# Optimization experiments

Measured on AMD Instinct MI355X. Metric: run time of the kernel, lower is better.

Reference implementation:

```python
import jax, jax.numpy as jnp
import numpy as np

B, N, G, M = 16, 8192, 512, 32
ENC = 384   # encoder_dims
TRD = 384   # trans_dim (must equal ENC due to cls-pos concat)
EPS = 1e-5


def _fps(xyz, n_samples):
    # farthest point sampling: xyz [B,N,3] -> idx [B,n_samples] int32
    b, n, _ = xyz.shape
    def body(carry, _):
        dists, farthest = carry                       # [B,N], [B]
        centroid = jnp.take_along_axis(xyz, farthest[:, None, None], axis=1)  # [B,1,3]
        d = jnp.sum((xyz - centroid) ** 2, -1)        # [B,N]
        dists = jnp.minimum(dists, d)
        nxt = jnp.argmax(dists, -1).astype(jnp.int32)
        return (dists, nxt), farthest
    init = (jnp.full((b, n), 1e10, xyz.dtype), jnp.zeros((b,), jnp.int32))
    _, idxs = jax.lax.scan(body, init, None, length=n_samples)
    return idxs.T                                     # [B,n_samples]


def _group(pts):
    # FPS centers + kNN neighborhoods, neighborhood recentered on its center
    fps_idx = _fps(pts, G)                                    # [B,G]
    center = jax.vmap(lambda p, i: p[i])(pts, fps_idx)        # [B,G,3]
    d2 = jnp.sum((center[:, :, None, :] - pts[:, None, :, :]) ** 2, -1)  # [B,G,N]
    _, knn_idx = jax.lax.top_k(-d2, M)                        # [B,G,M]
    nbhd = jax.vmap(lambda p, i: p[i])(pts, knn_idx)          # [B,G,M,3]
    nbhd = nbhd - center[:, :, None, :]
    return nbhd, center


def _bn(x, g, b, m, v):
    return (x - m) * jax.lax.rsqrt(v + EPS) * g + b


def _forward(pts, W1, b1, g1, be1, m1, v1, W2, b2,
             W3, b3, g2, be2, m2, v2, W4, b4,
             Wp1, bp1, Wp2, bp2, cls_pos):
    nbhd, center = _group(pts)                                # [B,G,M,3], [B,G,3]
    # Encoder (Point-MAE, BN in eval mode)
    f = jnp.einsum('bgmc,cd->bgmd', nbhd, W1) + b1            # [B,G,M,128]
    f = jax.nn.relu(_bn(f, g1, be1, m1, v1))
    f = jnp.einsum('bgmc,cd->bgmd', f, W2) + b2               # [B,G,M,256]
    fg = jnp.max(f, axis=2, keepdims=True)                    # [B,G,1,256]
    f = jnp.concatenate([jnp.broadcast_to(fg, f.shape), f], -1)  # [B,G,M,512]
    f = jnp.einsum('bgmc,cd->bgmd', f, W3) + b3
    f = jax.nn.relu(_bn(f, g2, be2, m2, v2))
    f = jnp.einsum('bgmc,cd->bgmd', f, W4) + b4               # [B,G,M,ENC]
    x = jnp.max(f, axis=2)                                    # [B,G,ENC]
    # pos embed MLP on centers
    pos = jax.nn.gelu(center @ Wp1 + bp1) @ Wp2 + bp2         # [B,G,TRD]
    cls = jnp.broadcast_to(cls_pos, (pts.shape[0], 1, ENC))
    pos = jnp.concatenate([cls, pos], axis=1)                 # [B,G+1,TRD]
    return x, pos


def setup_inputs() -> dict:
    key = jax.random.key(0)
    ks = jax.random.split(key, 20)
    nrm = lambda k, s, sc: jax.random.normal(k, s, jnp.float32) * sc
    uni = lambda k, s: jax.random.uniform(k, s, jnp.float32, 0.5, 1.5)
    return {
        'pts': jax.random.normal(ks[0], (B, N, 3), jnp.float32),
        'W1': nrm(ks[1], (3, 128), 0.1), 'b1': jnp.zeros((128,), jnp.float32),
        'g1': uni(ks[2], (128,)), 'be1': nrm(ks[3], (128,), 0.1),
        'm1': nrm(ks[4], (128,), 0.1), 'v1': uni(ks[5], (128,)),
        'W2': nrm(ks[6], (128, 256), 0.05), 'b2': jnp.zeros((256,), jnp.float32),
        'W3': nrm(ks[7], (512, 512), 0.04), 'b3': jnp.zeros((512,), jnp.float32),
        'g2': uni(ks[8], (512,)), 'be2': nrm(ks[9], (512,), 0.1),
        'm2': nrm(ks[10], (512,), 0.1), 'v2': uni(ks[11], (512,)),
        'W4': nrm(ks[12], (512, ENC), 0.04), 'b4': jnp.zeros((ENC,), jnp.float32),
        'Wp1': nrm(ks[13], (3, 128), 0.1), 'bp1': jnp.zeros((128,), jnp.float32),
        'Wp2': nrm(ks[14], (128, TRD), 0.08), 'bp2': jnp.zeros((TRD,), jnp.float32),
        'cls_pos': nrm(ks[15], (1, 1, ENC), 0.02),
    }


def reference(pts, W1, b1, g1, be1, m1, v1, W2, b2, W3, b3, g2, be2, m2, v2,
              W4, b4, Wp1, bp1, Wp2, bp2, cls_pos):
    return _forward(pts, W1, b1, g1, be1, m1, v1, W2, b2, W3, b3, g2, be2,
                    m2, v2, W4, b4, Wp1, bp1, Wp2, bp2, cls_pos)
```

## Files before the change

### kernel.cpp

```cpp
#include <hip/hip_runtime.h>

typedef _Float16 f16;
typedef _Float16 f16x8 __attribute__((ext_vector_type(8)));
typedef float    f32x4 __attribute__((ext_vector_type(4)));
typedef float    f32x2 __attribute__((ext_vector_type(2)));

#define NB   16
#define NP   8192
#define NG   512
#define NM   32
#define ENC  384
#define NROWS (NB * NG * NM)

__device__ __forceinline__ void gl_lds16(const void* g, void* l) {
  __builtin_amdgcn_global_load_lds((const __attribute__((address_space(1))) unsigned int*)g,
                                   (__attribute__((address_space(3))) unsigned int*)l, 16, 0, 0);
}

__device__ __forceinline__ f32x2 pk_add(f32x2 a, f32x2 b) {
  f32x2 d;
  asm("v_pk_add_f32 %0, %1, %2" : "=v"(d) : "v"(a), "v"(b));
  return d;
}
__device__ __forceinline__ f32x2 pk_mul(f32x2 a, f32x2 b) {
  f32x2 d;
  asm("v_pk_mul_f32 %0, %1, %2" : "=v"(d) : "v"(a), "v"(b));
  return d;
}

__device__ __forceinline__ unsigned long long kmax(unsigned long long a, unsigned long long b) {
  return a > b ? a : b;
}
__device__ __forceinline__ unsigned long long kmin(unsigned long long a, unsigned long long b) {
  return a < b ? a : b;
}

template <int CTRL>
__device__ __forceinline__ unsigned long long dpp_kmax(unsigned long long k) {
  int lo = (int)(unsigned)(k & 0xFFFFFFFFull);
  int hi = (int)(unsigned)(k >> 32);
  int olo = __builtin_amdgcn_update_dpp(lo, lo, CTRL, 0xF, 0xF, false);
  int ohi = __builtin_amdgcn_update_dpp(hi, hi, CTRL, 0xF, 0xF, false);
  unsigned long long o = ((unsigned long long)(unsigned)ohi << 32) | (unsigned)olo;
  return kmax(k, o);
}
template <int CTRL>
__device__ __forceinline__ unsigned long long dpp_kmin(unsigned long long k) {
  int lo = (int)(unsigned)(k & 0xFFFFFFFFull);
  int hi = (int)(unsigned)(k >> 32);
  int olo = __builtin_amdgcn_update_dpp(lo, lo, CTRL, 0xF, 0xF, false);
  int ohi = __builtin_amdgcn_update_dpp(hi, hi, CTRL, 0xF, 0xF, false);
  unsigned long long o = ((unsigned long long)(unsigned)ohi << 32) | (unsigned)olo;
  return kmin(k, o);
}
__device__ __forceinline__ unsigned long long swz16_kmax(unsigned long long k) {
  int lo = (int)(unsigned)(k & 0xFFFFFFFFull);
  int hi = (int)(unsigned)(k >> 32);
  int olo = __builtin_amdgcn_ds_swizzle(lo, 0x401F);
  int ohi = __builtin_amdgcn_ds_swizzle(hi, 0x401F);
  unsigned long long o = ((unsigned long long)(unsigned)ohi << 32) | (unsigned)olo;
  return kmax(k, o);
}
__device__ __forceinline__ unsigned long long swz16_kmin(unsigned long long k) {
  int lo = (int)(unsigned)(k & 0xFFFFFFFFull);
  int hi = (int)(unsigned)(k >> 32);
  int olo = __builtin_amdgcn_ds_swizzle(lo, 0x401F);
  int ohi = __builtin_amdgcn_ds_swizzle(hi, 0x401F);
  unsigned long long o = ((unsigned long long)(unsigned)ohi << 32) | (unsigned)olo;
  return kmin(k, o);
}

#define DPP_QUAD_XOR1 0xB1
#define DPP_QUAD_XOR2 0x4E
#define DPP_HALF_MIRR 0x141
#define DPP_ROW_MIRR  0x140

__global__ __launch_bounds__(512) void fps_kernel(const float* __restrict__ pts,
                                                  float* __restrict__ centers) {
#pragma clang fp contract(off)
  const int b = blockIdx.x;
  const float* pb = pts + (size_t)b * NP * 3;
  const int t = threadIdx.x;
  const int lane = t & 63, wid = t >> 6;
  __shared__ float spx[NP], spy[NP], spz[NP];
  __shared__ unsigned long long swk[2][16];
  f32x2 px2[8], py2[8], pz2[8];
  float dd[16];
#pragma unroll
  for (int i = 0; i < 16; ++i) {
    int idx = t + i * 512;
    float x = pb[idx * 3 + 0], y = pb[idx * 3 + 1], z = pb[idx * 3 + 2];
    px2[i >> 1][i & 1] = x; py2[i >> 1][i & 1] = y; pz2[i >> 1][i & 1] = z;
    dd[i] = 1e10f;
    spx[idx] = x; spy[idx] = y; spz[idx] = z;
  }
  __syncthreads();
  float cx = spx[0], cy = spy[0], cz = spz[0];
  for (int g = 0; g < NG; ++g) {
    if (t == 0) {
      float* c = centers + ((size_t)b * NG + g) * 3;
      c[0] = cx; c[1] = cy; c[2] = cz;
    }
    f32x2 ncx = {-cx, -cx}, ncy = {-cy, -cy}, ncz = {-cz, -cz};
    float best = -1.0f; int bslot = 0;
#pragma unroll
    for (int p = 0; p < 8; ++p) {
      f32x2 dx = pk_add(px2[p], ncx);
      f32x2 dy = pk_add(py2[p], ncy);
      f32x2 dz = pk_add(pz2[p], ncz);
      f32x2 d2 = pk_add(pk_add(pk_mul(dx, dx), pk_mul(dy, dy)), pk_mul(dz, dz));
      dd[2 * p] = fminf(dd[2 * p], d2[0]);
      if (dd[2 * p] > best) { best = dd[2 * p]; bslot = 2 * p; }
      dd[2 * p + 1] = fminf(dd[2 * p + 1], d2[1]);
      if (dd[2 * p + 1] > best) { best = dd[2 * p + 1]; bslot = 2 * p + 1; }
    }
    int bidx = t + bslot * 512;
    unsigned long long key =
        ((unsigned long long)__float_as_uint(best) << 13) | (unsigned)(8191 - bidx);
    key = dpp_kmax<DPP_QUAD_XOR1>(key);
    key = dpp_kmax<DPP_QUAD_XOR2>(key);
    key = dpp_kmax<DPP_HALF_MIRR>(key);
    key = dpp_kmax<DPP_ROW_MIRR>(key);
    key = swz16_kmax(key);
    const int p = g & 1;
    if ((lane & 31) == 0) swk[p][wid * 2 + (lane >> 5)] = key;
    __syncthreads();
    unsigned long long k2 = swk[p][lane & 15];
    k2 = dpp_kmax<DPP_QUAD_XOR1>(k2);
    k2 = dpp_kmax<DPP_QUAD_XOR2>(k2);
    k2 = dpp_kmax<DPP_HALF_MIRR>(k2);
    k2 = dpp_kmax<DPP_ROW_MIRR>(k2);
    int widx = 8191 - (int)(k2 & 0x1FFFull);
    cx = spx[widx]; cy = spy[widx]; cz = spz[widx];
  }
}

__global__ __launch_bounds__(256) void knn_kernel(const float* __restrict__ pts,
                                                  const float* __restrict__ centers,
                                                  int* __restrict__ knn_idx) {
#pragma clang fp contract(off)
  const int gg = blockIdx.x;
  const int b = gg >> 9;
  const float* pb = pts + (size_t)b * NP * 3;
  const float* c = centers + (size_t)gg * 3;
  const float cx = c[0], cy = c[1], cz = c[2];
  __shared__ unsigned long long swk[2][8];
  const int t = threadIdx.x, lane = t & 63, wid = t >> 6;
  float d[32];
  float lmin = 3e38f; int lidx = 0;
#pragma unroll
  for (int i = 0; i < 32; ++i) {
    int idx = i * 256 + t;
    float dx = __fsub_rn(cx, pb[idx * 3 + 0]);
    float dy = __fsub_rn(cy, pb[idx * 3 + 1]);
    float dz = __fsub_rn(cz, pb[idx * 3 + 2]);
    d[i] = __fadd_rn(__fadd_rn(__fmul_rn(dx, dx), __fmul_rn(dy, dy)), __fmul_rn(dz, dz));
    if (d[i] < lmin) { lmin = d[i]; lidx = idx; }
  }
  int* outp = knn_idx + (size_t)gg * NM;
  for (int r = 0; r < NM; ++r) {
    unsigned long long key =
        ((unsigned long long)__float_as_uint(lmin) << 13) | (unsigned)lidx;
    key = dpp_kmin<DPP_QUAD_XOR1>(key);
    key = dpp_kmin<DPP_QUAD_XOR2>(key);
    key = dpp_kmin<DPP_HALF_MIRR>(key);
    key = dpp_kmin<DPP_ROW_MIRR>(key);
    key = swz16_kmin(key);
    const int p = r & 1;
    if ((lane & 31) == 0) swk[p][wid * 2 + (lane >> 5)] = key;
    __syncthreads();
    unsigned long long k2 = swk[p][lane & 7];
    k2 = dpp_kmin<DPP_QUAD_XOR1>(k2);
    k2 = dpp_kmin<DPP_QUAD_XOR2>(k2);
    k2 = dpp_kmin<DPP_HALF_MIRR>(k2);
    int i0 = (int)(k2 & 0x1FFFull);
    if (t == 0) outp[r] = i0;
    if ((i0 & 255) == t) {
      int slot = i0 >> 8;
      lmin = 3e38f; lidx = 0;
#pragma unroll
      for (int i = 0; i < 32; ++i) {
        float di = (i == slot) ? 3e38f : d[i];
        d[i] = di;
        if (di < lmin) { lmin = di; lidx = i * 256 + t; }
      }
    }
  }
}

__global__ void quant_kernel(const float* __restrict__ W2, const float* __restrict__ W3,
                             const float* __restrict__ W4, const float* __restrict__ Wp2,
                             const float* __restrict__ b1, const float* __restrict__ g1,
                             const float* __restrict__ be1, const float* __restrict__ m1,
                             const float* __restrict__ v1, const float* __restrict__ g2,
                             const float* __restrict__ be2, const float* __restrict__ m2,
                             const float* __restrict__ v2,
                             f16* __restrict__ W2T, f16* __restrict__ W3aT,
                             f16* __restrict__ W3bT, f16* __restrict__ W4T,
                             f16* __restrict__ Wp2T,
                             float* __restrict__ s1, float* __restrict__ sh1,
                             float* __restrict__ s2, float* __restrict__ sh2) {
  int i = blockIdx.x * 256 + threadIdx.x;
  if (i < 32768) { int n = i >> 7, k = i & 127; W2T[i] = (f16)W2[(size_t)k * 256 + n]; return; }
  i -= 32768;
  if (i < 131072) { int n = i >> 8, k = i & 255; W3aT[i] = (f16)W3[(size_t)k * 512 + n]; return; }
  i -= 131072;
  if (i < 131072) { int n = i >> 8, k = i & 255; W3bT[i] = (f16)W3[(size_t)(256 + k) * 512 + n]; return; }
  i -= 131072;
  if (i < 196608) { int n = i >> 9, k = i & 511; W4T[i] = (f16)W4[(size_t)k * 384 + n]; return; }
  i -= 196608;
  if (i < 49152) { int n = i >> 7, k = i & 127; Wp2T[i] = (f16)Wp2[(size_t)k * 384 + n]; return; }
  i -= 49152;
  if (i < 128) {
    float s = g1[i] * rsqrtf(v1[i] + 1e-5f);
    s1[i] = s; sh1[i] = (b1[i] - m1[i]) * s + be1[i];
    return;
  }
  i -= 128;
  if (i < 512) {
    float s = g2[i] * rsqrtf(v2[i] + 1e-5f);
    s2[i] = s; sh2[i] = be2[i] - m2[i] * s;
    return;
  }
}

template <int WRITE_F2>
__global__ __launch_bounds__(256) void l2f_kernel(const float* __restrict__ pts,
                                                  const float* __restrict__ centers,
                                                  const int* __restrict__ knn_idx,
                                                  const float* __restrict__ W1,
                                                  const float* __restrict__ s1,
                                                  const float* __restrict__ sh1,
                                                  const f16* __restrict__ W2T,
                                                  const float* __restrict__ b2,
                                                  f16* __restrict__ fg,
                                                  f16* __restrict__ f2, int grow0) {
  __shared__ __align__(16) f16 sF1[128 * 128];
  __shared__ float snb[128][3];
  const int t = threadIdx.x, lane = t & 63, wid = t >> 6;
  const int wr = wid >> 1, wc = wid & 1;
  const int l15 = lane & 15, lhi = lane >> 4;
  const int grow = grow0 + blockIdx.x * 128;
  const int y = blockIdx.y;

  if (t < 128) {
    int row = grow + t;
    int gg = row >> 5;
    int b = gg >> 9;
    int idx = knn_idx[(size_t)gg * NM + (row & 31)];
    const float* p = pts + ((size_t)b * NP + idx) * 3;
    const float* c = centers + (size_t)gg * 3;
    snb[t][0] = p[0] - c[0];
    snb[t][1] = p[1] - c[1];
    snb[t][2] = p[2] - c[2];
  }
  __syncthreads();
  {
    int row = t >> 1, c0 = (t & 1) * 64;
    float nx = snb[row][0], ny = snb[row][1], nz = snb[row][2];
    int sw = (row & 7) << 4;
#pragma unroll
    for (int cc = 0; cc < 64; cc += 8) {
      f16x8 v;
#pragma unroll
      for (int j = 0; j < 8; ++j) {
        int c = c0 + cc + j;
        float a = nx * W1[c] + ny * W1[128 + c] + nz * W1[256 + c];
        a = a * s1[c] + sh1[c];
        v[j] = (f16)fmaxf(a, 0.0f);
      }
      *(f16x8*)((char*)sF1 + row * 256 + (((c0 + cc) * 2) ^ sw)) = v;
    }
  }
  __syncthreads();

  f32x4 acc[4][4];
#pragma unroll
  for (int m = 0; m < 4; ++m)
#pragma unroll
    for (int n = 0; n < 4; ++n) acc[m][n] = (f32x4){0.f, 0.f, 0.f, 0.f};

  const f16* Wb = W2T + (size_t)(y * 128) * 128;
#pragma unroll
  for (int ks = 0; ks < 4; ++ks) {
    f16x8 af[4], bf[4];
#pragma unroll
    for (int m = 0; m < 4; ++m) {
      int row = wr * 64 + m * 16 + l15;
      af[m] = *(const f16x8*)((const char*)sF1 + row * 256 + ((ks * 64 + lhi * 16) ^ ((row & 7) << 4)));
    }
#pragma unroll
    for (int n = 0; n < 4; ++n) {
      int nr = wc * 64 + n * 16 + l15;
      bf[n] = *(const f16x8*)(Wb + (size_t)nr * 128 + ks * 32 + lhi * 8);
    }
#pragma unroll
    for (int m = 0; m < 4; ++m)
#pragma unroll
      for (int n = 0; n < 4; ++n)
        acc[m][n] = __builtin_amdgcn_mfma_f32_16x16x32_f16(af[m], bf[n], acc[m][n], 0, 0, 0);
  }

  float bias[4];
#pragma unroll
  for (int n = 0; n < 4; ++n) bias[n] = b2[y * 128 + wc * 64 + n * 16 + l15];
#pragma unroll
  for (int p = 0; p < 2; ++p) {
#pragma unroll
    for (int n = 0; n < 4; ++n) {
      float v = acc[2 * p][n][0];
#pragma unroll
      for (int i = 1; i < 4; ++i) v = fmaxf(v, acc[2 * p][n][i]);
#pragma unroll
      for (int i = 0; i < 4; ++i) v = fmaxf(v, acc[2 * p + 1][n][i]);
      v = fmaxf(v, __shfl_xor(v, 16));
      v = fmaxf(v, __shfl_xor(v, 32));
      if (lhi == 0)
        fg[(size_t)((grow >> 5) + wr * 2 + p) * 256 + y * 128 + wc * 64 + n * 16 + l15] =
            (f16)(v + bias[n]);
    }
  }

  if (WRITE_F2) {
    __syncthreads();
    f16* sF2 = sF1;
#pragma unroll
    for (int n = 0; n < 4; ++n) {
      int col = wc * 64 + n * 16 + l15;
#pragma unroll
      for (int m = 0; m < 4; ++m)
#pragma unroll
        for (int i = 0; i < 4; ++i) {
          int row = wr * 64 + m * 16 + lhi * 4 + i;
          sF2[row * 128 + col] = (f16)(acc[m][n][i] + bias[n]);
        }
    }
    __syncthreads();
#pragma unroll
    for (int ch = 0; ch < 8; ++ch) {
      int off = ch * 4096 + t * 16;
      int row = off >> 8, cb = off & 255;
      *(uint4*)((char*)f2 + (size_t)(blockIdx.x * 128 + row) * 512 + y * 256 + cb) =
          *(const uint4*)((const char*)sF2 + off);
    }
  }
}

template <int K, int EPI>
__global__ __launch_bounds__(256) void gemm128_kernel(const f16* __restrict__ A,
                                                      const f16* __restrict__ BT,
                                                      float* __restrict__ outF32,
                                                      f16* __restrict__ outF16,
                                                      const float* __restrict__ e0,
                                                      const float* __restrict__ e1,
                                                      const float* __restrict__ e2,
                                                      int NTOT, int gg0) {
  __shared__ __align__(16) f16 sA[128 * 64];
  __shared__ __align__(16) f16 sB[128 * 64];
  const int t = threadIdx.x, lane = t & 63, wid = t >> 6;
  const int wrow = wid >> 1, wcol = wid & 1;
  const int l15 = lane & 15, lhi = lane >> 4;
  f32x4 acc[4][4];
#pragma unroll
  for (int m = 0; m < 4; ++m)
#pragma unroll
    for (int n = 0; n < 4; ++n) acc[m][n] = (f32x4){0.f, 0.f, 0.f, 0.f};

  const size_t arow0 = (size_t)blockIdx.x * 128;
  const int ncol0 = blockIdx.y * 128;
  const char* Ab = (const char*)A;
  const char* Bb = (const char*)BT;
  const int so = wid * 1024 + lane * 16;
  const int cb = so & 127;
  const int r0 = so >> 7;

  for (int kt = 0; kt < K; kt += 64) {
#pragma unroll
    for (int rnd = 0; rnd < 4; ++rnd) {
      int r = rnd * 32 + r0;
      int sw = (r & 7) << 4;
      gl_lds16(Ab + (arow0 + r) * (size_t)(K * 2) + kt * 2 + (cb ^ sw),
               (char*)sA + rnd * 4096 + wid * 1024);
      gl_lds16(Bb + (size_t)(ncol0 + r) * (K * 2) + kt * 2 + (cb ^ sw),
               (char*)sB + rnd * 4096 + wid * 1024);
    }
    __syncthreads();
#pragma unroll
    for (int ks = 0; ks < 2; ++ks) {
      f16x8 af[4], bf[4];
#pragma unroll
      for (int m = 0; m < 4; ++m) {
        int row = wrow * 64 + m * 16 + l15;
        int addr = row * 128 + ((ks * 64 + lhi * 16) ^ ((row & 7) << 4));
        af[m] = *(const f16x8*)((const char*)sA + addr);
      }
#pragma unroll
      for (int n = 0; n < 4; ++n) {
        int nrow = wcol * 64 + n * 16 + l15;
        int addr = nrow * 128 + ((ks * 64 + lhi * 16) ^ ((nrow & 7) << 4));
        bf[n] = *(const f16x8*)((const char*)sB + addr);
      }
#pragma unroll
      for (int m = 0; m < 4; ++m)
#pragma unroll
        for (int n = 0; n < 4; ++n)
          acc[m][n] = __builtin_amdgcn_mfma_f32_16x16x32_f16(af[m], bf[n], acc[m][n], 0, 0, 0);
    }
    __syncthreads();
  }

  if (EPI == 1) {
#pragma unroll
    for (int n = 0; n < 4; ++n) {
      int col = ncol0 + wcol * 64 + n * 16 + l15;
      float s = e1[col], sh = e2[col];
#pragma unroll
      for (int m = 0; m < 4; ++m) {
        int grp = gg0 + blockIdx.x * 4 + wrow * 2 + (m >> 1);
        float gv = e0[(size_t)grp * 512 + col];
#pragma unroll
        for (int i = 0; i < 4; ++i) {
          size_t row = arow0 + wrow * 64 + m * 16 + lhi * 4 + i;
          float v = (acc[m][n][i] + gv) * s + sh;
          outF16[row * NTOT + col] = (f16)fmaxf(v, 0.0f);
        }
      }
    }
  } else if (EPI == 2) {
#pragma unroll
    for (int pr = 0; pr < 2; ++pr) {
      size_t gg_glob = (size_t)gg0 + blockIdx.x * 4 + wrow * 2 + pr;
#pragma unroll
      for (int n = 0; n < 4; ++n) {
        float v = acc[2 * pr][n][0];
#pragma unroll
        for (int i = 1; i < 4; ++i) v = fmaxf(v, acc[2 * pr][n][i]);
#pragma unroll
        for (int i = 0; i < 4; ++i) v = fmaxf(v, acc[2 * pr + 1][n][i]);
        v = fmaxf(v, __shfl_xor(v, 16));
        v = fmaxf(v, __shfl_xor(v, 32));
        if (lhi == 0) {
          int col = ncol0 + wcol * 64 + n * 16 + l15;
          outF32[gg_glob * ENC + col] = v + e0[col];
        }
      }
    }
  } else if (EPI == 3) {
#pragma unroll
    for (int n = 0; n < 4; ++n) {
      int col = ncol0 + wcol * 64 + n * 16 + l15;
      float bias = e0[col];
#pragma unroll
      for (int m = 0; m < 4; ++m)
#pragma unroll
        for (int i = 0; i < 4; ++i) {
          size_t row = arow0 + wrow * 64 + m * 16 + lhi * 4 + i;
          outF32[row * NTOT + col] = acc[m][n][i] + bias;
        }
    }
  } else {
#pragma unroll
    for (int n = 0; n < 4; ++n) {
      int col = ncol0 + wcol * 64 + n * 16 + l15;
      float bias = e0[col];
#pragma unroll
      for (int m = 0; m < 4; ++m)
#pragma unroll
        for (int i = 0; i < 4; ++i) {
          size_t row = arow0 + wrow * 64 + m * 16 + lhi * 4 + i;
          int b = (int)(row >> 9), g = (int)(row & 511);
          outF32[((size_t)b * 513 + 1 + g) * 384 + col] = acc[m][n][i] + bias;
        }
    }
  }
}

__global__ __launch_bounds__(256) void posh_kernel(const float* __restrict__ centers,
                                                   const float* __restrict__ Wp1,
                                                   const float* __restrict__ bp1,
                                                   f16* __restrict__ h) {
  int o = blockIdx.x * 256 + threadIdx.x;
  int row = o >> 7, c = o & 127;
  const float* ct = centers + (size_t)row * 3;
  float x = ct[0] * Wp1[c] + ct[1] * Wp1[128 + c] + ct[2] * Wp1[256 + c] + bp1[c];
  float u = 0.7978845608028654f * (x + 0.044715f * x * x * x);
  h[o] = (f16)(0.5f * x * (1.0f + tanhf(u)));
}

__global__ void cls_kernel(const float* __restrict__ cls_pos, float* __restrict__ out_pos) {
  out_pos[(size_t)blockIdx.x * (NG + 1) * ENC + threadIdx.x] = cls_pos[threadIdx.x];
}

extern "C" void kernel_launch(void* const* d_in, const int* in_sizes, int n_in,
                              void* d_out, int out_size, void* d_ws, size_t ws_size,
                              hipStream_t stream) {
  const float* pts = (const float*)d_in[0];
  const float* W1  = (const float*)d_in[1];
  const float* b1  = (const float*)d_in[2];
  const float* g1  = (const float*)d_in[3];
  const float* be1 = (const float*)d_in[4];
  const float* m1  = (const float*)d_in[5];
  const float* v1  = (const float*)d_in[6];
  const float* W2  = (const float*)d_in[7];
  const float* b2  = (const float*)d_in[8];
  const float* W3  = (const float*)d_in[9];
  const float* b3  = (const float*)d_in[10];
  const float* g2  = (const float*)d_in[11];
  const float* be2 = (const float*)d_in[12];
  const float* m2  = (const float*)d_in[13];
  const float* v2  = (const float*)d_in[14];
  const float* W4  = (const float*)d_in[15];
  const float* b4  = (const float*)d_in[16];
  const float* Wp1 = (const float*)d_in[17];
  const float* bp1 = (const float*)d_in[18];
  const float* Wp2 = (const float*)d_in[19];
  const float* bp2 = (const float*)d_in[20];
  const float* cls = (const float*)d_in[21];

  float* out_x   = (float*)d_out;
  float* out_pos = out_x + (size_t)NB * NG * ENC;

  char* w = (char*)d_ws;
  auto alloc = [&](size_t bytes) {
    char* p = w;
    w += (bytes + 255) & ~(size_t)255;
    return p;
  };
  float* centers = (float*)alloc((size_t)NB * NG * 3 * 4);
  int*   knn     = (int*)alloc((size_t)NB * NG * NM * 4);
  f16*   W2T     = (f16*)alloc(32768 * 2);
  f16*   W3aT    = (f16*)alloc(131072 * 2);
  f16*   W3bT    = (f16*)alloc(131072 * 2);
  f16*   W4T     = (f16*)alloc(196608 * 2);
  f16*   Wp2T    = (f16*)alloc(49152 * 2);
  float* s1      = (float*)alloc(128 * 4);
  float* sh1     = (float*)alloc(128 * 4);
  float* s2      = (float*)alloc(512 * 4);
  float* sh2     = (float*)alloc(512 * 4);
  f16*   fg      = (f16*)alloc((size_t)8192 * 256 * 2);
  float* g3      = (float*)alloc((size_t)8192 * 512 * 4);
  f16*   h       = (f16*)alloc((size_t)8192 * 128 * 2);
  size_t fixed = (size_t)(w - (char*)d_ws);
  const size_t f2_full = (size_t)NROWS * 256 * 2;
  const size_t f3_full = (size_t)NROWS * 512 * 2;

  quant_kernel<<<dim3(2115), dim3(256), 0, stream>>>(W2, W3, W4, Wp2, b1, g1, be1, m1, v1,
                                                     g2, be2, m2, v2, W2T, W3aT, W3bT, W4T,
                                                     Wp2T, s1, sh1, s2, sh2);
  fps_kernel<<<dim3(NB), dim3(512), 0, stream>>>(pts, centers);
  knn_kernel<<<dim3(NB * NG), dim3(256), 0, stream>>>(pts, centers, knn);

  if (ws_size >= fixed + f2_full + f3_full + 4096) {
    f16* f2 = (f16*)alloc(f2_full);
    f16* f3 = (f16*)alloc(f3_full);
    l2f_kernel<1><<<dim3(2048, 2), dim3(256), 0, stream>>>(pts, centers, knn, W1, s1, sh1,
                                                           W2T, b2, fg, f2, 0);
    gemm128_kernel<256, 3><<<dim3(64, 4), dim3(256), 0, stream>>>(
        fg, W3aT, g3, nullptr, b3, nullptr, nullptr, 512, 0);
    gemm128_kernel<256, 1><<<dim3(2048, 4), dim3(256), 0, stream>>>(
        f2, W3bT, nullptr, f3, g3, s2, sh2, 512, 0);
    gemm128_kernel<512, 2><<<dim3(2048, 3), dim3(256), 0, stream>>>(
        f3, W4T, out_x, nullptr, b4, nullptr, nullptr, 384, 0);
  } else if (ws_size >= fixed + f2_full + f3_full / 4 + 4096) {
    f16* f2 = (f16*)alloc(f2_full);
    f16* f3c = (f16*)alloc(f3_full / 4);
    l2f_kernel<1><<<dim3(2048, 2), dim3(256), 0, stream>>>(pts, centers, knn, W1, s1, sh1,
                                                           W2T, b2, fg, f2, 0);
    gemm128_kernel<256, 3><<<dim3(64, 4), dim3(256), 0, stream>>>(
        fg, W3aT, g3, nullptr, b3, nullptr, nullptr, 512, 0);
    for (int c = 0; c < 4; ++c) {
      gemm128_kernel<256, 1><<<dim3(512, 4), dim3(256), 0, stream>>>(
          f2 + (size_t)c * 65536 * 256, W3bT, nullptr, f3c, g3, s2, sh2, 512, c * 2048);
      gemm128_kernel<512, 2><<<dim3(512, 3), dim3(256), 0, stream>>>(
          f3c, W4T, out_x, nullptr, b4, nullptr, nullptr, 384, c * 2048);
    }
  } else {
    f16* f2c = (f16*)alloc((size_t)32768 * 256 * 2);
    f16* f3c = (f16*)alloc((size_t)32768 * 512 * 2);
    l2f_kernel<0><<<dim3(2048, 2), dim3(256), 0, stream>>>(pts, centers, knn, W1, s1, sh1,
                                                           W2T, b2, fg, nullptr, 0);
    gemm128_kernel<256, 3><<<dim3(64, 4), dim3(256), 0, stream>>>(
        fg, W3aT, g3, nullptr, b3, nullptr, nullptr, 512, 0);
    for (int c = 0; c < 8; ++c) {
      l2f_kernel<1><<<dim3(256, 2), dim3(256), 0, stream>>>(pts, centers, knn, W1, s1, sh1,
                                                            W2T, b2, fg, f2c, c * 32768);
      gemm128_kernel<256, 1><<<dim3(256, 4), dim3(256), 0, stream>>>(
          f2c, W3bT, nullptr, f3c, g3, s2, sh2, 512, c * 1024);
      gemm128_kernel<512, 2><<<dim3(256, 3), dim3(256), 0, stream>>>(
          f3c, W4T, out_x, nullptr, b4, nullptr, nullptr, 384, c * 1024);
    }
  }

  posh_kernel<<<dim3(4096), dim3(256), 0, stream>>>(centers, Wp1, bp1, h);
  gemm128_kernel<128, 4><<<dim3(64, 3), dim3(256), 0, stream>>>(
      h, Wp2T, out_pos, nullptr, bp2, nullptr, nullptr, 384, 0);
  cls_kernel<<<dim3(NB), dim3(ENC), 0, stream>>>(cls, out_pos);
}
```

Measured before the change: 1.194 ms.

## Tree-reduce FPS argmax, use DPP row broadcasts, and chunk encoder GEMMs

```diff
diff --git a/kernel.cpp b/kernel.cpp
--- a/kernel.cpp
+++ b/kernel.cpp
@@ -53,14 +53,6 @@
   unsigned long long o = ((unsigned long long)(unsigned)ohi << 32) | (unsigned)olo;
   return kmin(k, o);
 }
-__device__ __forceinline__ unsigned long long swz16_kmax(unsigned long long k) {
-  int lo = (int)(unsigned)(k & 0xFFFFFFFFull);
-  int hi = (int)(unsigned)(k >> 32);
-  int olo = __builtin_amdgcn_ds_swizzle(lo, 0x401F);
-  int ohi = __builtin_amdgcn_ds_swizzle(hi, 0x401F);
-  unsigned long long o = ((unsigned long long)(unsigned)ohi << 32) | (unsigned)olo;
-  return kmax(k, o);
-}
 __device__ __forceinline__ unsigned long long swz16_kmin(unsigned long long k) {
   int lo = (int)(unsigned)(k & 0xFFFFFFFFull);
   int hi = (int)(unsigned)(k >> 32);
@@ -74,6 +66,8 @@
 #define DPP_QUAD_XOR2 0x4E
 #define DPP_HALF_MIRR 0x141
 #define DPP_ROW_MIRR  0x140
+#define DPP_BCAST15   0x142
+#define DPP_BCAST31   0x143
 
 __global__ __launch_bounds__(512) void fps_kernel(const float* __restrict__ pts,
                                                   float* __restrict__ centers) {
@@ -83,7 +77,7 @@
   const int t = threadIdx.x;
   const int lane = t & 63, wid = t >> 6;
   __shared__ float spx[NP], spy[NP], spz[NP];
-  __shared__ unsigned long long swk[2][16];
+  __shared__ unsigned long long swk[2][8];
   f32x2 px2[8], py2[8], pz2[8];
   float dd[16];
 #pragma unroll
@@ -102,34 +96,55 @@
       c[0] = cx; c[1] = cy; c[2] = cz;
     }
     f32x2 ncx = {-cx, -cx}, ncy = {-cy, -cy}, ncz = {-cz, -cz};
-    float best = -1.0f; int bslot = 0;
 #pragma unroll
     for (int p = 0; p < 8; ++p) {
       f32x2 dx = pk_add(px2[p], ncx);
       f32x2 dy = pk_add(py2[p], ncy);
       f32x2 dz = pk_add(pz2[p], ncz);
       f32x2 d2 = pk_add(pk_add(pk_mul(dx, dx), pk_mul(dy, dy)), pk_mul(dz, dz));
-      dd[2 * p] = fminf(dd[2 * p], d2[0]);
-      if (dd[2 * p] > best) { best = dd[2 * p]; bslot = 2 * p; }
+      dd[2 * p]     = fminf(dd[2 * p], d2[0]);
       dd[2 * p + 1] = fminf(dd[2 * p + 1], d2[1]);
-      if (dd[2 * p + 1] > best) { best = dd[2 * p + 1]; bslot = 2 * p + 1; }
-    }
-    int bidx = t + bslot * 512;
+    }
+    float tv[8]; int ti[8];
+#pragma unroll
+    for (int i = 0; i < 8; ++i) {
+      bool gt = dd[2 * i + 1] > dd[2 * i];
+      tv[i] = gt ? dd[2 * i + 1] : dd[2 * i];
+      ti[i] = gt ? 2 * i + 1 : 2 * i;
+    }
+#pragma unroll
+    for (int i = 0; i < 4; ++i) {
+      bool gt = tv[2 * i + 1] > tv[2 * i];
+      tv[i] = gt ? tv[2 * i + 1] : tv[2 * i];
+      ti[i] = gt ? ti[2 * i + 1] : ti[2 * i];
+    }
+    {
+      bool gt = tv[1] > tv[0];
+      tv[0] = gt ? tv[1] : tv[0];
+      ti[0] = gt ? ti[1] : ti[0];
+      gt = tv[3] > tv[2];
+      tv[1] = gt ? tv[3] : tv[2];
+      ti[1] = gt ? ti[3] : ti[2];
+      gt = tv[1] > tv[0];
+      tv[0] = gt ? tv[1] : tv[0];
+      ti[0] = gt ? ti[1] : ti[0];
+    }
+    int bidx = t + ti[0] * 512;
     unsigned long long key =
-        ((unsigned long long)__float_as_uint(best) << 13) | (unsigned)(8191 - bidx);
+        ((unsigned long long)__float_as_uint(tv[0]) << 13) | (unsigned)(8191 - bidx);
     key = dpp_kmax<DPP_QUAD_XOR1>(key);
     key = dpp_kmax<DPP_QUAD_XOR2>(key);
     key = dpp_kmax<DPP_HALF_MIRR>(key);
     key = dpp_kmax<DPP_ROW_MIRR>(key);
-    key = swz16_kmax(key);
+    key = dpp_kmax<DPP_BCAST15>(key);
+    key = dpp_kmax<DPP_BCAST31>(key);
     const int p = g & 1;
-    if ((lane & 31) == 0) swk[p][wid * 2 + (lane >> 5)] = key;
+    if (lane == 63) swk[p][wid] = key;
     __syncthreads();
-    unsigned long long k2 = swk[p][lane & 15];
+    unsigned long long k2 = swk[p][lane & 7];
     k2 = dpp_kmax<DPP_QUAD_XOR1>(k2);
     k2 = dpp_kmax<DPP_QUAD_XOR2>(k2);
     k2 = dpp_kmax<DPP_HALF_MIRR>(k2);
-    k2 = dpp_kmax<DPP_ROW_MIRR>(k2);
     int widx = 8191 - (int)(k2 & 0x1FFFull);
     cx = spx[widx]; cy = spy[widx]; cz = spz[widx];
   }
@@ -550,19 +565,8 @@
   fps_kernel<<<dim3(NB), dim3(512), 0, stream>>>(pts, centers);
   knn_kernel<<<dim3(NB * NG), dim3(256), 0, stream>>>(pts, centers, knn);
 
-  if (ws_size >= fixed + f2_full + f3_full + 4096) {
-    f16* f2 = (f16*)alloc(f2_full);
-    f16* f3 = (f16*)alloc(f3_full);
-    l2f_kernel<1><<<dim3(2048, 2), dim3(256), 0, stream>>>(pts, centers, knn, W1, s1, sh1,
-                                                           W2T, b2, fg, f2, 0);
-    gemm128_kernel<256, 3><<<dim3(64, 4), dim3(256), 0, stream>>>(
-        fg, W3aT, g3, nullptr, b3, nullptr, nullptr, 512, 0);
-    gemm128_kernel<256, 1><<<dim3(2048, 4), dim3(256), 0, stream>>>(
-        f2, W3bT, nullptr, f3, g3, s2, sh2, 512, 0);
-    gemm128_kernel<512, 2><<<dim3(2048, 3), dim3(256), 0, stream>>>(
-        f3, W4T, out_x, nullptr, b4, nullptr, nullptr, 384, 0);
-  } else if (ws_size >= fixed + f2_full + f3_full / 4 + 4096) {
-    f16* f2 = (f16*)alloc(f2_full);
+  if (ws_size >= fixed + f2_full + f3_full / 4 + 4096) {
+    f16* f2  = (f16*)alloc(f2_full);
     f16* f3c = (f16*)alloc(f3_full / 4);
     l2f_kernel<1><<<dim3(2048, 2), dim3(256), 0, stream>>>(pts, centers, knn, W1, s1, sh1,
                                                            W2T, b2, fg, f2, 0);
```

Result: slower. 1.315 ms (+10.1%).

## Fuse encoder layer-3 and layer-4 GEMMs into one kernel keeping f3 in LDS

Applied to the files above, without the earlier changes.

```diff
diff --git a/kernel.cpp b/kernel.cpp
--- a/kernel.cpp
+++ b/kernel.cpp
@@ -346,15 +346,140 @@
   }
 }
 
+__global__ __launch_bounds__(256) void l34_kernel(const f16* __restrict__ f2,
+                                                  const f16* __restrict__ W3bT,
+                                                  const f16* __restrict__ W4T,
+                                                  const float* __restrict__ g3,
+                                                  const float* __restrict__ s2v,
+                                                  const float* __restrict__ sh2v,
+                                                  const float* __restrict__ b4,
+                                                  float* __restrict__ out_x,
+                                                  int gg0) {
+  __shared__ __align__(16) char sMem[65536];
+  char* sA  = sMem;
+  char* sB  = sMem + 32768;
+  char* sF3 = sMem + 49152;
+  const int t = threadIdx.x, lane = t & 63, wid = t >> 6;
+  const int wr = wid >> 1, wc = wid & 1;
+  const int l15 = lane & 15, lhi = lane >> 4;
+  const int row0 = blockIdx.x * 64;
+  const int ggb = gg0 + (row0 >> 5);
+
+#pragma unroll
+  for (int rnd = 0; rnd < 8; ++rnd) {
+    int o = rnd * 4096 + t * 16;
+    int row = o >> 9, cb = o & 511;
+    gl_lds16((const char*)f2 + (size_t)(row0 + row) * 512 + (cb ^ ((row & 7) << 4)), sA + o);
+  }
+
+  f32x4 acc2[2][12];
+#pragma unroll
+  for (int m = 0; m < 2; ++m)
+#pragma unroll
+    for (int n = 0; n < 12; ++n) acc2[m][n] = (f32x4){0.f, 0.f, 0.f, 0.f};
+
+  for (int j = 0; j < 4; ++j) {
+    f32x4 acc1[2][4];
+#pragma unroll
+    for (int m = 0; m < 2; ++m)
+#pragma unroll
+      for (int n = 0; n < 4; ++n) acc1[m][n] = (f32x4){0.f, 0.f, 0.f, 0.f};
+
+    for (int kt = 0; kt < 4; ++kt) {
+#pragma unroll
+      for (int rnd = 0; rnd < 4; ++rnd) {
+        int o = rnd * 4096 + t * 16;
+        int brow = o >> 7, bcol = o & 127;
+        gl_lds16((const char*)W3bT + (size_t)(j * 128 + brow) * 512 + kt * 128 +
+                     (bcol ^ ((brow & 7) << 4)),
+                 sB + o);
+      }
+      __syncthreads();
+#pragma unroll
+      for (int ks = 0; ks < 2; ++ks) {
+        f16x8 af[2], bf[4];
+#pragma unroll
+        for (int m = 0; m < 2; ++m) {
+          int row = wr * 32 + m * 16 + l15;
+          af[m] = *(const f16x8*)(sA + row * 512 +
+                                  ((kt * 128 + ks * 64 + lhi * 16) ^ ((row & 7) << 4)));
+        }
+#pragma unroll
+        for (int n = 0; n < 4; ++n) {
+          int br = wc * 64 + n * 16 + l15;
+          bf[n] = *(const f16x8*)(sB + br * 128 + ((ks * 64 + lhi * 16) ^ ((br & 7) << 4)));
+        }
+#pragma unroll
+        for (int m = 0; m < 2; ++m)
+#pragma unroll
+          for (int n = 0; n < 4; ++n)
+            acc1[m][n] = __builtin_amdgcn_mfma_f32_16x16x32_f16(af[m], bf[n], acc1[m][n], 0, 0, 0);
+      }
+      __syncthreads();
+    }
+
+    {
+      int grp = ggb + wr;
+#pragma unroll
+      for (int n = 0; n < 4; ++n) {
+        int col = wc * 64 + n * 16 + l15;
+        int gc = j * 128 + col;
+        float s = s2v[gc], sh = sh2v[gc];
+        float gv = g3[(size_t)grp * 512 + gc];
+#pragma unroll
+        for (int m = 0; m < 2; ++m)
+#pragma unroll
+          for (int i = 0; i < 4; ++i) {
+            int row = wr * 32 + m * 16 + lhi * 4 + i;
+            float v = (acc1[m][n][i] + gv) * s + sh;
+            *(f16*)(sF3 + row * 256 + ((col * 2) ^ ((row & 7) << 4))) = (f16)fmaxf(v, 0.0f);
+          }
+      }
+    }
+    __syncthreads();
+
+#pragma unroll
+    for (int ks = 0; ks < 4; ++ks) {
+      f16x8 af[2];
+#pragma unroll
+      for (int m = 0; m < 2; ++m) {
+        int row = wr * 32 + m * 16 + l15;
+        af[m] = *(const f16x8*)(sF3 + row * 256 + ((ks * 64 + lhi * 16) ^ ((row & 7) << 4)));
+      }
+#pragma unroll
+      for (int n = 0; n < 12; ++n) {
+        int nrow = wc * 192 + n * 16 + l15;
+        f16x8 bf = *(const f16x8*)((const char*)W4T + (size_t)nrow * 1024 +
+                                   (j * 128 + ks * 32 + lhi * 8) * 2);
+        acc2[0][n] = __builtin_amdgcn_mfma_f32_16x16x32_f16(af[0], bf, acc2[0][n], 0, 0, 0);
+        acc2[1][n] = __builtin_amdgcn_mfma_f32_16x16x32_f16(af[1], bf, acc2[1][n], 0, 0, 0);
+      }
+    }
+  }
+
+  size_t gout = (size_t)(ggb + wr) * ENC;
+#pragma unroll
+  for (int n = 0; n < 12; ++n) {
+    float v = acc2[0][n][0];
+#pragma unroll
+    for (int i = 1; i < 4; ++i) v = fmaxf(v, acc2[0][n][i]);
+#pragma unroll
+    for (int i = 0; i < 4; ++i) v = fmaxf(v, acc2[1][n][i]);
+    v = fmaxf(v, __shfl_xor(v, 16));
+    v = fmaxf(v, __shfl_xor(v, 32));
+    if (lhi == 0) {
+      int col = wc * 192 + n * 16 + l15;
+      out_x[gout + col] = v + b4[col];
+    }
+  }
+}
+
 template <int K, int EPI>
 __global__ __launch_bounds__(256) void gemm128_kernel(const f16* __restrict__ A,
                                                       const f16* __restrict__ BT,
                                                       float* __restrict__ outF32,
-                                                      f16* __restrict__ outF16,
                                                       const float* __restrict__ e0,
-                                                      const float* __restrict__ e1,
-                                                      const float* __restrict__ e2,
-                                                      int NTOT, int gg0) {
+                                                      int NTOT) {
   __shared__ __align__(16) f16 sA[128 * 64];
   __shared__ __align__(16) f16 sB[128 * 64];
   const int t = threadIdx.x, lane = t & 63, wid = t >> 6;
@@ -409,43 +534,7 @@
     __syncthreads();
   }
 
-  if (EPI == 1) {
-#pragma unroll
-    for (int n = 0; n < 4; ++n) {
-      int col = ncol0 + wcol * 64 + n * 16 + l15;
-      float s = e1[col], sh = e2[col];
-#pragma unroll
-      for (int m = 0; m < 4; ++m) {
-        int grp = gg0 + blockIdx.x * 4 + wrow * 2 + (m >> 1);
-        float gv = e0[(size_t)grp * 512 + col];
-#pragma unroll
-        for (int i = 0; i < 4; ++i) {
-          size_t row = arow0 + wrow * 64 + m * 16 + lhi * 4 + i;
-          float v = (acc[m][n][i] + gv) * s + sh;
-          outF16[row * NTOT + col] = (f16)fmaxf(v, 0.0f);
-        }
-      }
-    }
-  } else if (EPI == 2) {
-#pragma unroll
-    for (int pr = 0; pr < 2; ++pr) {
-      size_t gg_glob = (size_t)gg0 + blockIdx.x * 4 + wrow * 2 + pr;
-#pragma unroll
-      for (int n = 0; n < 4; ++n) {
-        float v = acc[2 * pr][n][0];
-#pragma unroll
-        for (int i = 1; i < 4; ++i) v = fmaxf(v, acc[2 * pr][n][i]);
-#pragma unroll
-        for (int i = 0; i < 4; ++i) v = fmaxf(v, acc[2 * pr + 1][n][i]);
-        v = fmaxf(v, __shfl_xor(v, 16));
-        v = fmaxf(v, __shfl_xor(v, 32));
-        if (lhi == 0) {
-          int col = ncol0 + wcol * 64 + n * 16 + l15;
-          outF32[gg_glob * ENC + col] = v + e0[col];
-        }
-      }
-    }
-  } else if (EPI == 3) {
+  if (EPI == 3) {
 #pragma unroll
     for (int n = 0; n < 4; ++n) {
       int col = ncol0 + wcol * 64 + n * 16 + l15;
@@ -542,7 +631,6 @@
   f16*   h       = (f16*)alloc((size_t)8192 * 128 * 2);
   size_t fixed = (size_t)(w - (char*)d_ws);
   const size_t f2_full = (size_t)NROWS * 256 * 2;
-  const size_t f3_full = (size_t)NROWS * 512 * 2;
 
   quant_kernel<<<dim3(2115), dim3(256), 0, stream>>>(W2, W3, W4, Wp2, b1, g1, be1, m1, v1,
                                                      g2, be2, m2, v2, W2T, W3aT, W3bT, W4T,
@@ -550,49 +638,27 @@
   fps_kernel<<<dim3(NB), dim3(512), 0, stream>>>(pts, centers);
   knn_kernel<<<dim3(NB * NG), dim3(256), 0, stream>>>(pts, centers, knn);
 
-  if (ws_size >= fixed + f2_full + f3_full + 4096) {
+  if (ws_size >= fixed + f2_full + 4096) {
     f16* f2 = (f16*)alloc(f2_full);
-    f16* f3 = (f16*)alloc(f3_full);
     l2f_kernel<1><<<dim3(2048, 2), dim3(256), 0, stream>>>(pts, centers, knn, W1, s1, sh1,
                                                            W2T, b2, fg, f2, 0);
-    gemm128_kernel<256, 3><<<dim3(64, 4), dim3(256), 0, stream>>>(
-        fg, W3aT, g3, nullptr, b3, nullptr, nullptr, 512, 0);
-    gemm128_kernel<256, 1><<<dim3(2048, 4), dim3(256), 0, stream>>>(
-        f2, W3bT, nullptr, f3, g3, s2, sh2, 512, 0);
-    gemm128_kernel<512, 2><<<dim3(2048, 3), dim3(256), 0, stream>>>(
-        f3, W4T, out_x, nullptr, b4, nullptr, nullptr, 384, 0);
-  } else if (ws_size >= fixed + f2_full + f3_full / 4 + 4096) {
-    f16* f2 = (f16*)alloc(f2_full);
-    f16* f3c = (f16*)alloc(f3_full / 4);
-    l2f_kernel<1><<<dim3(2048, 2), dim3(256), 0, stream>>>(pts, centers, knn, W1, s1, sh1,
-                                                           W2T, b2, fg, f2, 0);
-    gemm128_kernel<256, 3><<<dim3(64, 4), dim3(256), 0, stream>>>(
-        fg, W3aT, g3, nullptr, b3, nullptr, nullptr, 512, 0);
-    for (int c = 0; c < 4; ++c) {
-      gemm128_kernel<256, 1><<<dim3(512, 4), dim3(256), 0, stream>>>(
-          f2 + (size_t)c * 65536 * 256, W3bT, nullptr, f3c, g3, s2, sh2, 512, c * 2048);
-      gemm128_kernel<512, 2><<<dim3(512, 3), dim3(256), 0, stream>>>(
-          f3c, W4T, out_x, nullptr, b4, nullptr, nullptr, 384, c * 2048);
-    }
+    gemm128_kernel<256, 3><<<dim3(64, 4), dim3(256), 0, stream>>>(fg, W3aT, g3, b3, 512);
+    l34_kernel<<<dim3(NROWS / 64), dim3(256), 0, stream>>>(f2, W3bT, W4T, g3, s2, sh2, b4,
+                                                           out_x, 0);
   } else {
     f16* f2c = (f16*)alloc((size_t)32768 * 256 * 2);
-    f16* f3c = (f16*)alloc((size_t)32768 * 512 * 2);
     l2f_kernel<0><<<dim3(2048, 2), dim3(256), 0, stream>>>(pts, centers, knn, W1, s1, sh1,
                                                            W2T, b2, fg, nullptr, 0);
-    gemm128_kernel<256, 3><<<dim3(64, 4), dim3(256), 0, stream>>>(
-        fg, W3aT, g3, nullptr, b3, nullptr, nullptr, 512, 0);
+    gemm128_kernel<256, 3><<<dim3(64, 4), dim3(256), 0, stream>>>(fg, W3aT, g3, b3, 512);
     for (int c = 0; c < 8; ++c) {
       l2f_kernel<1><<<dim3(256, 2), dim3(256), 0, stream>>>(pts, centers, knn, W1, s1, sh1,
                                                             W2T, b2, fg, f2c, c * 32768);
-      gemm128_kernel<256, 1><<<dim3(256, 4), dim3(256), 0, stream>>>(
-          f2c, W3bT, nullptr, f3c, g3, s2, sh2, 512, c * 1024);
-      gemm128_kernel<512, 2><<<dim3(256, 3), dim3(256), 0, stream>>>(
-          f3c, W4T, out_x, nullptr, b4, nullptr, nullptr, 384, c * 1024);
+      l34_kernel<<<dim3(512), dim3(256), 0, stream>>>(f2c, W3bT, W4T, g3, s2, sh2, b4,
+                                                      out_x, c * 1024);
     }
   }
 
   posh_kernel<<<dim3(4096), dim3(256), 0, stream>>>(centers, Wp1, bp1, h);
-  gemm128_kernel<128, 4><<<dim3(64, 3), dim3(256), 0, stream>>>(
-      h, Wp2T, out_pos, nullptr, bp2, nullptr, nullptr, 384, 0);
+  gemm128_kernel<128, 4><<<dim3(64, 3), dim3(256), 0, stream>>>(h, Wp2T, out_pos, bp2, 384);
   cls_kernel<<<dim3(NB), dim3(ENC), 0, stream>>>(cls, out_pos);
 }
```

Measured after the change: 1.481 ms. 24.0% more time.
